# Kernel optimization log

Hardware: AMD Instinct MI355X
Metric: run time of the kernel (lower is better)

## Reference

```python
import jax, jax.numpy as jnp
import numpy as np
from jax import lax

B = 2; H = 32; W = 32; C = 384
NH = 12; NG = 6; KK = 7; STRIDE = 1; ORF = 2.0
CG = C // NG; HC = C // NH; GH = NH // NG; HID = 4 * C
EPS = 1e-5


def layernorm(x, w, b):
    mu = jnp.mean(x, axis=-1, keepdims=True)
    var = jnp.mean((x - mu) ** 2, axis=-1, keepdims=True)
    return (x - mu) * lax.rsqrt(var + EPS) * w + b


def ref_points(Hk, Wk):
    # normalized reference grid in (-1,1), ordering (y, x) as in _get_ref_points
    ry = ((jnp.arange(Hk, dtype=jnp.float32) + 0.5) / Hk) * 2.0 - 1.0
    rx = ((jnp.arange(Wk, dtype=jnp.float32) + 0.5) / Wk) * 2.0 - 1.0
    return jnp.stack(jnp.meshgrid(ry, rx, indexing='ij'), axis=-1)  # (Hk, Wk, 2)


def grid_sample(img, grid):
    # torch F.grid_sample: bilinear, align_corners=True, padding_mode='zeros'
    # img: (N, Cc, Hi, Wi); grid: (N, ..., 2) with (x, y) in [-1, 1]
    N, Cc, Hi, Wi = img.shape
    out_shape = grid.shape[1:-1]
    g = grid.reshape(N, -1, 2)
    x = (g[..., 0] + 1.0) * 0.5 * (Wi - 1)
    y = (g[..., 1] + 1.0) * 0.5 * (Hi - 1)
    x0 = jnp.floor(x); y0 = jnp.floor(y)
    wx1 = x - x0; wy1 = y - y0
    flat = img.reshape(N, Cc, Hi * Wi)
    M = g.shape[1]
    def gather(ix, iy, wgt):
        valid = (ix >= 0) & (ix <= Wi - 1) & (iy >= 0) & (iy <= Hi - 1)
        idx = (jnp.clip(iy, 0, Hi - 1) * Wi + jnp.clip(ix, 0, Wi - 1)).astype(jnp.int32)
        vals = jnp.take_along_axis(flat, jnp.broadcast_to(idx[:, None, :], (N, Cc, M)), axis=2)
        return vals * (wgt * valid.astype(img.dtype))[:, None, :]
    out = (gather(x0, y0, (1 - wx1) * (1 - wy1))
           + gather(x0 + 1, y0, wx1 * (1 - wy1))
           + gather(x0, y0 + 1, (1 - wx1) * wy1)
           + gather(x0 + 1, y0 + 1, wx1 * wy1))
    return out.reshape((N, Cc) + out_shape)


def setup_inputs() -> dict:
    ks = jax.random.split(jax.random.key(0), 16)
    n = lambda k, s, sc=0.02: jax.random.normal(k, s, jnp.float32) * sc
    return dict(
        x=jax.random.normal(ks[0], (B, H * W, C), jnp.float32),
        norm1_w=jnp.ones((C,), jnp.float32), norm1_b=jnp.zeros((C,), jnp.float32),
        wq=n(ks[1], (C, C)), bq=jnp.zeros((C,), jnp.float32),
        wk=n(ks[2], (C, C)), bk=jnp.zeros((C,), jnp.float32),
        wv=n(ks[3], (C, C)), bv=jnp.zeros((C,), jnp.float32),
        wo=n(ks[4], (C, C)), bo=jnp.zeros((C,), jnp.float32),
        off_dw_w=n(ks[5], (CG, 1, KK, KK)), off_dw_b=jnp.zeros((CG,), jnp.float32),
        off_ln_w=jnp.ones((CG,), jnp.float32), off_ln_b=jnp.zeros((CG,), jnp.float32),
        off_pw_w=n(ks[6], (2, CG)),
        rpe_table=n(ks[7], (NH, 2 * H - 1, 2 * W - 1), 0.01),
        norm2_w=jnp.ones((C,), jnp.float32), norm2_b=jnp.zeros((C,), jnp.float32),
        fc1_w=n(ks[8], (HID, C)), fc1_b=jnp.zeros((HID,), jnp.float32),
        fc2_w=n(ks[9], (C, HID)), fc2_b=jnp.zeros((C,), jnp.float32),
    )


def reference(x, norm1_w, norm1_b, wq, bq, wk, bk, wv, bv, wo, bo,
              off_dw_w, off_dw_b, off_ln_w, off_ln_b, off_pw_w, rpe_table,
              norm2_w, norm2_b, fc1_w, fc1_b, fc2_w, fc2_b):
    Bx, L, Cx = x.shape
    shortcut = x
    xn = layernorm(x, norm1_w, norm1_b)
    xi = xn.reshape(Bx, H, W, Cx).transpose(0, 3, 1, 2)  # (B, C, H, W)

    # proj_q (1x1 conv)
    q = jnp.einsum('bchw,dc->bdhw', xi, wq) + bq[None, :, None, None]

    # offset network on per-group channels
    q_off = q.reshape(Bx * NG, CG, H, W)
    o = lax.conv_general_dilated(q_off, off_dw_w, (STRIDE, STRIDE),
                                 [(KK // 2, KK // 2), (KK // 2, KK // 2)],
                                 dimension_numbers=('NCHW', 'OIHW', 'NCHW'),
                                 feature_group_count=CG) + off_dw_b[None, :, None, None]
    o = layernorm(o.transpose(0, 2, 3, 1), off_ln_w, off_ln_b)  # (Bg, Hk, Wk, CG)
    o = jax.nn.gelu(o, approximate=False)
    offset = jnp.einsum('bhwc,pc->bphw', o, off_pw_w)  # (Bg, 2, Hk, Wk)
    Hk, Wk = offset.shape[2], offset.shape[3]
    ns = Hk * Wk
    orange = jnp.array([1.0 / Hk, 1.0 / Wk], jnp.float32).reshape(1, 2, 1, 1)
    offset = jnp.tanh(offset) * orange * ORF
    offset = offset.transpose(0, 2, 3, 1)  # (Bg, Hk, Wk, 2) (y, x)
    pos = offset + ref_points(Hk, Wk)[None]  # offset_range_factor >= 0 branch

    # deformable sampling of the (normed) feature map
    xs = grid_sample(xi.reshape(Bx * NG, CG, H, W), pos[..., ::-1])  # (Bg, CG, Hk, Wk)
    xs = xs.reshape(Bx, Cx, 1, ns)

    k = (jnp.einsum('bcxn,dc->bdxn', xs, wk) + bk[None, :, None, None]).reshape(Bx * NH, HC, ns)
    v = (jnp.einsum('bcxn,dc->bdxn', xs, wv) + bv[None, :, None, None]).reshape(Bx * NH, HC, ns)
    q_ = q.reshape(Bx * NH, HC, H * W)

    attn = jnp.einsum('bcm,bcn->bmn', q_, k) * (HC ** -0.5)  # (B*NH, HW, ns)

    # continuous relative position bias via grid_sample on rpe_table
    rpe = jnp.broadcast_to(rpe_table[None], (Bx, NH, 2 * H - 1, 2 * W - 1)).reshape(
        Bx * NG, GH, 2 * H - 1, 2 * W - 1)
    qg = ref_points(H, W).reshape(H * W, 2)[None]  # (1, HW, 2)
    disp = (qg[:, :, None, :] - pos.reshape(Bx * NG, ns, 2)[:, None, :, :]) * 0.5  # (Bg, HW, ns, 2)
    bias = grid_sample(rpe, disp[..., ::-1])  # (Bg, GH, HW, ns)
    attn = attn + bias.reshape(Bx * NH, H * W, ns)

    attn = jax.nn.softmax(attn, axis=2)
    out = jnp.einsum('bmn,bcn->bcm', attn, v).reshape(Bx, Cx, H, W)
    y = jnp.einsum('bchw,dc->bdhw', out, wo) + bo[None, :, None, None]
    y = y.transpose(0, 2, 3, 1).reshape(Bx, L, Cx)

    x2 = shortcut + y
    h = layernorm(x2, norm2_w, norm2_b)
    h = jax.nn.gelu(h @ fc1_w.T + fc1_b, approximate=False) @ fc2_w.T + fc2_b
    return x2 + h
```

## Files before the change

### kernel.cpp

```cpp
#include <hip/hip_runtime.h>
#include <math.h>

#define Bc 2
#define Hh 32
#define Ww 32
#define Cc 384
#define NHc 12
#define NGc 6
#define CGc 64
#define HCc 32
#define GHc 2
#define HIDc 1536
#define Lc 1024
#define NSc 1024
#define BGc 12

typedef float f32x4 __attribute__((ext_vector_type(4)));
typedef short bf16x8 __attribute__((ext_vector_type(8)));

__device__ __forceinline__ float gelu_f(float v) {
    return 0.5f * v * (1.f + erff(v * 0.70710678118654752440f));
}

__device__ __forceinline__ unsigned short f2bf(float f) {
    unsigned u = __float_as_uint(f);
    u = (u + 0x7FFF + ((u >> 16) & 1)) >> 16;
    return (unsigned short)u;
}

__device__ __forceinline__ float bf2f(unsigned short u) {
    return __uint_as_float((unsigned)u << 16);
}

__global__ __launch_bounds__(128) void ln_kernel(
    const float* __restrict__ x, const float* __restrict__ w,
    const float* __restrict__ b, unsigned short* __restrict__ out)
{
    __shared__ float l1[2], l2[2];
    int row = blockIdx.x;
    int t = threadIdx.x;
    const float* xr = x + (size_t)row * Cc;
    float v0 = xr[t], v1 = xr[t + 128], v2 = xr[t + 256];
    float s = v0 + v1 + v2;
    #pragma unroll
    for (int o = 32; o; o >>= 1) s += __shfl_down(s, o);
    if ((t & 63) == 0) l1[t >> 6] = s;
    __syncthreads();
    float mu = (l1[0] + l1[1]) * (1.f / Cc);
    float d0 = v0 - mu, d1 = v1 - mu, d2 = v2 - mu;
    float q = d0 * d0 + d1 * d1 + d2 * d2;
    #pragma unroll
    for (int o = 32; o; o >>= 1) q += __shfl_down(q, o);
    if ((t & 63) == 0) l2[t >> 6] = q;
    __syncthreads();
    float rstd = rsqrtf((l2[0] + l2[1]) * (1.f / Cc) + 1e-5f);
    unsigned short* orow = out + (size_t)row * Cc;
    orow[t]       = f2bf(d0 * rstd * w[t]       + b[t]);
    orow[t + 128] = f2bf(d1 * rstd * w[t + 128] + b[t + 128]);
    orow[t + 256] = f2bf(d2 * rstd * w[t + 256] + b[t + 256]);
}

__global__ __launch_bounds__(256) void cast_kernel(
    const float* __restrict__ src, unsigned short* __restrict__ dst, int n)
{
    int i = blockIdx.x * 1024 + threadIdx.x * 4;
    if (i < n) {
        float4 v = *(const float4*)(src + i);
        ushort4 u;
        u.x = f2bf(v.x); u.y = f2bf(v.y); u.z = f2bf(v.z); u.w = f2bf(v.w);
        *(ushort4*)(dst + i) = u;
    }
}

template<int EPI>
__global__ __launch_bounds__(256) void mfma_gemm(
    const unsigned short* __restrict__ A, const unsigned short* __restrict__ W,
    const float* __restrict__ bias, const float* __restrict__ res,
    void* __restrict__ out1, void* __restrict__ out2, int M, int N, int K)
{
    int w = threadIdx.x >> 6, l = threadIdx.x & 63;
    int col = l & 15, quad = l >> 4;
    int mb = blockIdx.x * 64 + w * 16;
    int n0 = blockIdx.y * 64;
    const unsigned short* Ap = A + (size_t)(mb + col) * K + quad * 8;
    f32x4 acc[4] = {};
    for (int k0 = 0; k0 < K; k0 += 32) {
        bf16x8 af = *(const bf16x8*)(Ap + k0);
        #pragma unroll
        for (int ch = 0; ch < 4; ch++) {
            bf16x8 wf = *(const bf16x8*)(W + (size_t)(n0 + ch * 16 + col) * K + k0 + quad * 8);
            acc[ch] = __builtin_amdgcn_mfma_f32_16x16x32_bf16(af, wf, acc[ch], 0, 0, 0);
        }
    }
    int bb = mb >> 10, l0 = (mb & 1023) + quad * 4;
    #pragma unroll
    for (int ch = 0; ch < 4; ch++) {
        int n = n0 + ch * 16 + col;
        float bv = bias[n];
        if (EPI == 3) {
            float4 qv;
            qv.x = acc[ch][0] + bv; qv.y = acc[ch][1] + bv;
            qv.z = acc[ch][2] + bv; qv.w = acc[ch][3] + bv;
            *(float4*)&((float*)out1)[((size_t)(bb * Cc + n)) * Lc + l0] = qv;
            unsigned short* q2 = (unsigned short*)out2;
            size_t base = (((size_t)(bb * NHc + (n >> 5))) * Lc + l0) * 32 + (n & 31);
            q2[base]      = f2bf(qv.x);
            q2[base + 32] = f2bf(qv.y);
            q2[base + 64] = f2bf(qv.z);
            q2[base + 96] = f2bf(qv.w);
        } else if (EPI == 5) {
            ushort4 u;
            u.x = f2bf(acc[ch][0] + bv); u.y = f2bf(acc[ch][1] + bv);
            u.z = f2bf(acc[ch][2] + bv); u.w = f2bf(acc[ch][3] + bv);
            *(ushort4*)&((unsigned short*)out1)[((size_t)(bb * Cc + n)) * NSc + l0] = u;
        } else {
            #pragma unroll
            for (int r = 0; r < 4; r++) {
                size_t m = mb + quad * 4 + r;
                float v = acc[ch][r] + bv;
                if (EPI == 1)
                    ((unsigned short*)out1)[m * N + n] = f2bf(gelu_f(v));
                else if (EPI == 4)
                    ((unsigned short*)out1)[m * N + n] = f2bf(v);
                else
                    ((float*)out1)[m * N + n] = v + res[m * N + n];
            }
        }
    }
}

__global__ __launch_bounds__(256) void dwconv_kernel(
    const float* __restrict__ q, const float* __restrict__ wdw,
    const float* __restrict__ bdw, float* __restrict__ o_dw)
{
    int cg = blockIdx.x, bg = blockIdx.y;
    int b = bg / NGc, g = bg % NGc;
    __shared__ float wk_s[49];
    __shared__ float img[1024];
    const float* qp = q + (size_t)(b * Cc + g * CGc + cg) * Lc;
    if (threadIdx.x < 49) wk_s[threadIdx.x] = wdw[cg * 49 + threadIdx.x];
    #pragma unroll
    for (int i = 0; i < 4; i++) img[threadIdx.x + i * 256] = qp[threadIdx.x + i * 256];
    __syncthreads();
    float bias = bdw[cg];
    #pragma unroll
    for (int i = 0; i < 4; i++) {
        int hw = threadIdx.x + i * 256;
        int y = hw >> 5, xx = hw & 31;
        float acc = bias;
        #pragma unroll
        for (int ky = 0; ky < 7; ky++) {
            int yy = y + ky - 3;
            if (yy < 0 || yy > 31) continue;
            #pragma unroll
            for (int kx = 0; kx < 7; kx++) {
                int x2 = xx + kx - 3;
                if (x2 < 0 || x2 > 31) continue;
                acc += img[yy * 32 + x2] * wk_s[ky * 7 + kx];
            }
        }
        o_dw[(size_t)(bg * CGc + cg) * Lc + hw] = acc;
    }
}

__global__ __launch_bounds__(64) void offset_kernel(
    const float* __restrict__ o_dw, const float* __restrict__ lnw,
    const float* __restrict__ lnb, const float* __restrict__ pw,
    float* __restrict__ pos)
{
    int hw = blockIdx.x, bg = blockIdx.y;
    int cg = threadIdx.x;
    float v = o_dw[(size_t)(bg * CGc + cg) * Lc + hw];
    float s = v;
    #pragma unroll
    for (int o = 32; o; o >>= 1) s += __shfl_down(s, o);
    s = __shfl(s, 0, 64);
    float mu = s * (1.f / CGc);
    float d = v - mu;
    float q2 = d * d;
    #pragma unroll
    for (int o = 32; o; o >>= 1) q2 += __shfl_down(q2, o);
    q2 = __shfl(q2, 0, 64);
    float rstd = rsqrtf(q2 * (1.f / CGc) + 1e-5f);
    float t = d * rstd * lnw[cg] + lnb[cg];
    float gl = gelu_f(t);
    float sy = gl * pw[cg];
    float sx = gl * pw[CGc + cg];
    #pragma unroll
    for (int o = 32; o; o >>= 1) {
        sy += __shfl_down(sy, o);
        sx += __shfl_down(sx, o);
    }
    if (threadIdx.x == 0) {
        float offy = tanhf(sy) * 0.0625f;
        float offx = tanhf(sx) * 0.0625f;
        int y = hw >> 5, xx = hw & 31;
        pos[((size_t)bg * Lc + hw) * 2 + 0] = offy + ((y + 0.5f) * (2.f / Hh) - 1.f);
        pos[((size_t)bg * Lc + hw) * 2 + 1] = offx + ((xx + 0.5f) * (2.f / Ww) - 1.f);
    }
}

__global__ __launch_bounds__(256) void sample_kernel(
    const unsigned short* __restrict__ xn, const float* __restrict__ pos,
    unsigned short* __restrict__ xs)
{
    int cg = threadIdx.x & 63;
    int nl = threadIdx.x >> 6;
    int n = blockIdx.x * 4 + nl;
    int bg = blockIdx.y;
    int b = bg / NGc, g = bg % NGc;
    float py = pos[((size_t)bg * NSc + n) * 2 + 0];
    float px = pos[((size_t)bg * NSc + n) * 2 + 1];
    float fx = (px + 1.f) * 0.5f * 31.f;
    float fy = (py + 1.f) * 0.5f * 31.f;
    float x0f = floorf(fx), y0f = floorf(fy);
    int x0 = (int)x0f, y0 = (int)y0f;
    float wx1 = fx - x0f, wy1 = fy - y0f;
    float wx0 = 1.f - wx1, wy0 = 1.f - wy1;
    const unsigned short* base = xn + (size_t)(b * Lc) * Cc + g * CGc + cg;
    float acc = 0.f;
    if (y0 >= 0 && y0 <= 31) {
        if (x0 >= 0 && x0 <= 31) acc += bf2f(base[(size_t)(y0 * 32 + x0) * Cc]) * wx0 * wy0;
        if (x0 + 1 >= 0 && x0 + 1 <= 31) acc += bf2f(base[(size_t)(y0 * 32 + x0 + 1) * Cc]) * wx1 * wy0;
    }
    if (y0 + 1 >= 0 && y0 + 1 <= 31) {
        if (x0 >= 0 && x0 <= 31) acc += bf2f(base[(size_t)((y0 + 1) * 32 + x0) * Cc]) * wx0 * wy1;
        if (x0 + 1 >= 0 && x0 + 1 <= 31) acc += bf2f(base[(size_t)((y0 + 1) * 32 + x0 + 1) * Cc]) * wx1 * wy1;
    }
    xs[((size_t)(b * NSc) + n) * Cc + g * CGc + cg] = f2bf(acc);
}

__global__ __launch_bounds__(256) void attn_kernel(
    const unsigned short* __restrict__ qbf, const unsigned short* __restrict__ kbf,
    const unsigned short* __restrict__ vtb, const float* __restrict__ pos,
    const float* __restrict__ rpe, unsigned short* __restrict__ attno)
{
    __shared__ float rpe_s[63 * 65];
    __shared__ unsigned short p_bf[4][16 * 72];
    __shared__ float ml_s[4][2][16];
    float* o_s = rpe_s;

    int m0 = blockIdx.x * 16;
    int h = blockIdx.y, b = blockIdx.z;
    int tid = threadIdx.x;
    int w = tid >> 6, l = tid & 63;
    int col = l & 15, quad = l >> 4;

    const float* tb = rpe + (size_t)h * 3969;
    for (int i = tid; i < 63 * 65; i += 256) {
        int row = i / 65, cx = i - row * 65;
        rpe_s[i] = (cx < 63) ? tb[row * 63 + cx] : 0.f;
    }

    bf16x8 qfrag = *(const bf16x8*)(qbf +
        ((((size_t)(b * NHc + h)) * Lc + m0 + col) * 32 + quad * 8));

    float qgy = ((m0 >> 5) + 0.5f) * (2.f / 32.f) - 1.f;
    float qgx0 = (((m0 & 31) + quad * 4) + 0.5f) * (2.f / 32.f) - 1.f;

    const unsigned short* kb_ = kbf + (size_t)b * NSc * Cc + h * HCc;
    const unsigned short* vb_ = vtb + ((size_t)(b * Cc + h * HCc)) * NSc;
    const float2* pp = (const float2*)(pos + (size_t)(b * NGc + (h >> 1)) * NSc * 2);

    float run_m[4] = {-3.0e38f, -3.0e38f, -3.0e38f, -3.0e38f};
    float run_l[4] = {0.f, 0.f, 0.f, 0.f};
    f32x4 O0 = {0.f, 0.f, 0.f, 0.f};
    f32x4 O1 = {0.f, 0.f, 0.f, 0.f};

    __syncthreads();

    for (int it = 0; it < 4; it++) {
        int n0 = w * 256 + it * 64;
        f32x4 s[4];
        #pragma unroll
        for (int ch = 0; ch < 4; ch++) {
            bf16x8 kf = *(const bf16x8*)(kb_ +
                ((size_t)(n0 + ch * 16 + col) * Cc + quad * 8));
            f32x4 z = {0.f, 0.f, 0.f, 0.f};
            s[ch] = __builtin_amdgcn_mfma_f32_16x16x32_bf16(qfrag, kf, z, 0, 0, 0);
        }
        #pragma unroll
        for (int ch = 0; ch < 4; ch++) {
            int n = n0 + ch * 16 + col;
            float2 pyx = pp[n];
            float fy = ((qgy - pyx.x) * 0.5f + 1.f) * 31.f;
            float y0f = floorf(fy);
            int iy = (int)y0f;
            float wy1 = fy - y0f, wy0 = 1.f - wy1;
            bool y0ok = (unsigned)iy <= 62u;
            bool y1ok = (unsigned)(iy + 1) <= 62u;
            const float* r0 = rpe_s + iy * 65;
            float fx0 = ((qgx0 - pyx.y) * 0.5f + 1.f) * 31.f;
            #pragma unroll
            for (int r = 0; r < 4; r++) {
                float fx = fx0 + r * 0.96875f;
                float x0f = floorf(fx);
                int ix = (int)x0f;
                float wx1 = fx - x0f, wx0 = 1.f - wx1;
                bool x0ok = (unsigned)ix <= 62u;
                bool x1ok = (unsigned)(ix + 1) <= 62u;
                float bias = 0.f;
                if (y0ok) {
                    if (x0ok) bias += r0[ix] * wy0 * wx0;
                    if (x1ok) bias += r0[ix + 1] * wy0 * wx1;
                }
                if (y1ok) {
                    if (x0ok) bias += r0[65 + ix] * wy1 * wx0;
                    if (x1ok) bias += r0[65 + ix + 1] * wy1 * wx1;
                }
                s[ch][r] = s[ch][r] * 0.17677669529663688f + bias;
            }
        }
        float nm[4], alpha[4];
        #pragma unroll
        for (int r = 0; r < 4; r++) {
            float mx = fmaxf(fmaxf(s[0][r], s[1][r]), fmaxf(s[2][r], s[3][r]));
            #pragma unroll
            for (int msk = 1; msk < 16; msk <<= 1)
                mx = fmaxf(mx, __shfl_xor(mx, msk));
            nm[r] = fmaxf(run_m[r], mx);
            alpha[r] = expf(run_m[r] - nm[r]);
            run_m[r] = nm[r];
        }
        float rowsum[4] = {0.f, 0.f, 0.f, 0.f};
        #pragma unroll
        for (int ch = 0; ch < 4; ch++)
            #pragma unroll
            for (int r = 0; r < 4; r++) {
                float e = expf(s[ch][r] - nm[r]);
                s[ch][r] = e;
                rowsum[r] += e;
            }
        #pragma unroll
        for (int r = 0; r < 4; r++) {
            float sm = rowsum[r];
            #pragma unroll
            for (int msk = 1; msk < 16; msk <<= 1)
                sm += __shfl_xor(sm, msk);
            run_l[r] = run_l[r] * alpha[r] + sm;
        }
        #pragma unroll
        for (int ch = 0; ch < 4; ch++)
            #pragma unroll
            for (int r = 0; r < 4; r++)
                p_bf[w][(quad * 4 + r) * 72 + ch * 16 + col] = f2bf(s[ch][r]);
        #pragma unroll
        for (int r = 0; r < 4; r++) { O0[r] *= alpha[r]; O1[r] *= alpha[r]; }
        #pragma unroll
        for (int half = 0; half < 2; half++) {
            bf16x8 pf = *(const bf16x8*)&p_bf[w][col * 72 + half * 32 + quad * 8];
            bf16x8 v0 = *(const bf16x8*)(vb_ +
                ((size_t)col * NSc + n0 + half * 32 + quad * 8));
            O0 = __builtin_amdgcn_mfma_f32_16x16x32_bf16(pf, v0, O0, 0, 0, 0);
            bf16x8 v1 = *(const bf16x8*)(vb_ +
                ((size_t)(col + 16) * NSc + n0 + half * 32 + quad * 8));
            O1 = __builtin_amdgcn_mfma_f32_16x16x32_bf16(pf, v1, O1, 0, 0, 0);
        }
    }
    __syncthreads();
    #pragma unroll
    for (int r = 0; r < 4; r++) {
        int m = quad * 4 + r;
        o_s[w * 528 + m * 33 + col] = O0[r];
        o_s[w * 528 + m * 33 + col + 16] = O1[r];
    }
    if (col == 0) {
        #pragma unroll
        for (int r = 0; r < 4; r++) {
            ml_s[w][0][quad * 4 + r] = run_m[r];
            ml_s[w][1][quad * 4 + r] = run_l[r];
        }
    }
    __syncthreads();
    for (int i = tid; i < 512; i += 256) {
        int m = i >> 5, c = i & 31;
        float fm = fmaxf(fmaxf(ml_s[0][0][m], ml_s[1][0][m]),
                         fmaxf(ml_s[2][0][m], ml_s[3][0][m]));
        float lsum = 0.f, osum = 0.f;
        #pragma unroll
        for (int ww = 0; ww < 4; ww++) {
            float sc = expf(ml_s[ww][0][m] - fm);
            lsum += ml_s[ww][1][m] * sc;
            osum += o_s[ww * 528 + m * 33 + c] * sc;
        }
        attno[((size_t)(b * Lc) + m0 + m) * Cc + h * HCc + c] = f2bf(osum / lsum);
    }
}

extern "C" void kernel_launch(void* const* d_in, const int* in_sizes, int n_in,
                              void* d_out, int out_size, void* d_ws, size_t ws_size,
                              hipStream_t stream)
{
    const float* x    = (const float*)d_in[0];
    const float* n1w  = (const float*)d_in[1];
    const float* n1b  = (const float*)d_in[2];
    const float* wq   = (const float*)d_in[3];
    const float* bq   = (const float*)d_in[4];
    const float* wk   = (const float*)d_in[5];
    const float* bk   = (const float*)d_in[6];
    const float* wv   = (const float*)d_in[7];
    const float* bv   = (const float*)d_in[8];
    const float* wo   = (const float*)d_in[9];
    const float* bo   = (const float*)d_in[10];
    const float* dw_w = (const float*)d_in[11];
    const float* dw_b = (const float*)d_in[12];
    const float* lnw  = (const float*)d_in[13];
    const float* lnb  = (const float*)d_in[14];
    const float* pw_w = (const float*)d_in[15];
    const float* rpe  = (const float*)d_in[16];
    const float* n2w  = (const float*)d_in[17];
    const float* n2b  = (const float*)d_in[18];
    const float* fc1w = (const float*)d_in[19];
    const float* fc1b = (const float*)d_in[20];
    const float* fc2w = (const float*)d_in[21];
    const float* fc2b = (const float*)d_in[22];
    float* out = (float*)d_out;

    float* ws = (float*)d_ws;
    unsigned short* xnbf = (unsigned short*)ws;
    float*          qb   = ws + 393216;
    unsigned short* qbf  = (unsigned short*)(ws + 1179648);
    unsigned short* h1bf = (unsigned short*)ws;
    float* odw   = ws + 1572864;
    unsigned short* xln2bf = (unsigned short*)(ws + 1572864);
    float* posb  = ws + 2359296;
    unsigned short* xsbf = (unsigned short*)(ws + 2383872);
    unsigned short* kbf  = (unsigned short*)(ws + 2777088);
    unsigned short* vtb  = (unsigned short*)(ws + 3170304);
    unsigned short* attnbf = (unsigned short*)(ws + 3563520);
    float* x2    = ws + 3956736;
    unsigned short* wqbf   = (unsigned short*)(ws + 4743168);
    unsigned short* wkbf   = (unsigned short*)(ws + 4816896);
    unsigned short* wvbf   = (unsigned short*)(ws + 4890624);
    unsigned short* wobf   = (unsigned short*)(ws + 4964352);
    unsigned short* fc1wbf = (unsigned short*)(ws + 5038080);
    unsigned short* fc2wbf = (unsigned short*)(ws + 5332992);

    cast_kernel<<<(Cc * Cc + 1023) / 1024, 256, 0, stream>>>(wq, wqbf, Cc * Cc);
    cast_kernel<<<(Cc * Cc + 1023) / 1024, 256, 0, stream>>>(wk, wkbf, Cc * Cc);
    cast_kernel<<<(Cc * Cc + 1023) / 1024, 256, 0, stream>>>(wv, wvbf, Cc * Cc);
    cast_kernel<<<(Cc * Cc + 1023) / 1024, 256, 0, stream>>>(wo, wobf, Cc * Cc);
    cast_kernel<<<(Cc * HIDc + 1023) / 1024, 256, 0, stream>>>(fc1w, fc1wbf, Cc * HIDc);
    cast_kernel<<<(Cc * HIDc + 1023) / 1024, 256, 0, stream>>>(fc2w, fc2wbf, Cc * HIDc);
    ln_kernel<<<Bc * Lc, 128, 0, stream>>>(x, n1w, n1b, xnbf);
    mfma_gemm<3><<<dim3(Bc * Lc / 64, Cc / 64), 256, 0, stream>>>(
        xnbf, wqbf, bq, x, qb, qbf, Bc * Lc, Cc, Cc);
    dwconv_kernel<<<dim3(CGc, BGc), 256, 0, stream>>>(qb, dw_w, dw_b, odw);
    offset_kernel<<<dim3(Lc, BGc), 64, 0, stream>>>(odw, lnw, lnb, pw_w, posb);
    sample_kernel<<<dim3(NSc / 4, BGc), 256, 0, stream>>>(xnbf, posb, xsbf);
    mfma_gemm<4><<<dim3(Bc * NSc / 64, Cc / 64), 256, 0, stream>>>(
        xsbf, wkbf, bk, x, kbf, kbf, Bc * NSc, Cc, Cc);
    mfma_gemm<5><<<dim3(Bc * NSc / 64, Cc / 64), 256, 0, stream>>>(
        xsbf, wvbf, bv, x, vtb, vtb, Bc * NSc, Cc, Cc);
    attn_kernel<<<dim3(Lc / 16, NHc, Bc), 256, 0, stream>>>(
        qbf, kbf, vtb, posb, rpe, attnbf);
    mfma_gemm<2><<<dim3(Bc * Lc / 64, Cc / 64), 256, 0, stream>>>(
        attnbf, wobf, bo, x, x2, x2, Bc * Lc, Cc, Cc);
    ln_kernel<<<Bc * Lc, 128, 0, stream>>>(x2, n2w, n2b, xln2bf);
    mfma_gemm<1><<<dim3(Bc * Lc / 64, HIDc / 64), 256, 0, stream>>>(
        xln2bf, fc1wbf, fc1b, x2, h1bf, h1bf, Bc * Lc, HIDc, Cc);
    mfma_gemm<2><<<dim3(Bc * Lc / 64, Cc / 64), 256, 0, stream>>>(
        h1bf, fc2wbf, fc2b, x2, out, out, Bc * Lc, Cc, HIDc);
}
```

Measured before the change: 331.8 us.

## Fuse weight casts and K/V GEMMs, narrow GEMM tiles, bf16 exp2 RPE table

Merges the six weight-cast launches into one kernel and fuses the K and V projections into a single MFMA kernel that shares the A-fragment load. Generic GEMM N-tiles are halved to 32 columns to double the grid, and offset_kernel now packs four positions per 256-thread block. The attention kernel stores the RPE table in shared memory as bf16 pre-scaled by log2(e) and uses exp2f, cutting LDS footprint and exp cost. The bf16 RPE values add some precision loss in the bias.

```diff
diff --git a/kernel.cpp b/kernel.cpp
--- a/kernel.cpp
+++ b/kernel.cpp
@@ -60,16 +60,27 @@
     orow[t + 256] = f2bf(d2 * rstd * w[t + 256] + b[t + 256]);
 }
 
-__global__ __launch_bounds__(256) void cast_kernel(
-    const float* __restrict__ src, unsigned short* __restrict__ dst, int n)
-{
-    int i = blockIdx.x * 1024 + threadIdx.x * 4;
-    if (i < n) {
-        float4 v = *(const float4*)(src + i);
-        ushort4 u;
-        u.x = f2bf(v.x); u.y = f2bf(v.y); u.z = f2bf(v.z); u.w = f2bf(v.w);
-        *(ushort4*)(dst + i) = u;
-    }
+__global__ __launch_bounds__(256) void cast6_kernel(
+    const float* __restrict__ wq, const float* __restrict__ wk,
+    const float* __restrict__ wv, const float* __restrict__ wo,
+    const float* __restrict__ f1, const float* __restrict__ f2,
+    unsigned short* __restrict__ dq, unsigned short* __restrict__ dk,
+    unsigned short* __restrict__ dv, unsigned short* __restrict__ d_o,
+    unsigned short* __restrict__ d1, unsigned short* __restrict__ d2)
+{
+    int bid = blockIdx.x;
+    const float* s; unsigned short* d; int base;
+    if (bid < 144)       { s = wq; d = dq;  base = bid; }
+    else if (bid < 288)  { s = wk; d = dk;  base = bid - 144; }
+    else if (bid < 432)  { s = wv; d = dv;  base = bid - 288; }
+    else if (bid < 576)  { s = wo; d = d_o; base = bid - 432; }
+    else if (bid < 1152) { s = f1; d = d1;  base = bid - 576; }
+    else                 { s = f2; d = d2;  base = bid - 1152; }
+    int i = base * 1024 + threadIdx.x * 4;
+    float4 v = *(const float4*)(s + i);
+    ushort4 u;
+    u.x = f2bf(v.x); u.y = f2bf(v.y); u.z = f2bf(v.z); u.w = f2bf(v.w);
+    *(ushort4*)(d + i) = u;
 }
 
 template<int EPI>
@@ -81,20 +92,22 @@
     int w = threadIdx.x >> 6, l = threadIdx.x & 63;
     int col = l & 15, quad = l >> 4;
     int mb = blockIdx.x * 64 + w * 16;
-    int n0 = blockIdx.y * 64;
+    int n0 = blockIdx.y * 32;
     const unsigned short* Ap = A + (size_t)(mb + col) * K + quad * 8;
-    f32x4 acc[4] = {};
+    const unsigned short* Wp0 = W + (size_t)(n0 + col) * K + quad * 8;
+    const unsigned short* Wp1 = W + (size_t)(n0 + 16 + col) * K + quad * 8;
+    f32x4 acc[2] = {};
+    #pragma unroll 4
     for (int k0 = 0; k0 < K; k0 += 32) {
         bf16x8 af = *(const bf16x8*)(Ap + k0);
-        #pragma unroll
-        for (int ch = 0; ch < 4; ch++) {
-            bf16x8 wf = *(const bf16x8*)(W + (size_t)(n0 + ch * 16 + col) * K + k0 + quad * 8);
-            acc[ch] = __builtin_amdgcn_mfma_f32_16x16x32_bf16(af, wf, acc[ch], 0, 0, 0);
-        }
+        bf16x8 w0 = *(const bf16x8*)(Wp0 + k0);
+        bf16x8 w1 = *(const bf16x8*)(Wp1 + k0);
+        acc[0] = __builtin_amdgcn_mfma_f32_16x16x32_bf16(af, w0, acc[0], 0, 0, 0);
+        acc[1] = __builtin_amdgcn_mfma_f32_16x16x32_bf16(af, w1, acc[1], 0, 0, 0);
     }
     int bb = mb >> 10, l0 = (mb & 1023) + quad * 4;
     #pragma unroll
-    for (int ch = 0; ch < 4; ch++) {
+    for (int ch = 0; ch < 2; ch++) {
         int n = n0 + ch * 16 + col;
         float bv = bias[n];
         if (EPI == 3) {
@@ -108,11 +121,6 @@
             q2[base + 32] = f2bf(qv.y);
             q2[base + 64] = f2bf(qv.z);
             q2[base + 96] = f2bf(qv.w);
-        } else if (EPI == 5) {
-            ushort4 u;
-            u.x = f2bf(acc[ch][0] + bv); u.y = f2bf(acc[ch][1] + bv);
-            u.z = f2bf(acc[ch][2] + bv); u.w = f2bf(acc[ch][3] + bv);
-            *(ushort4*)&((unsigned short*)out1)[((size_t)(bb * Cc + n)) * NSc + l0] = u;
         } else {
             #pragma unroll
             for (int r = 0; r < 4; r++) {
@@ -120,12 +128,53 @@
                 float v = acc[ch][r] + bv;
                 if (EPI == 1)
                     ((unsigned short*)out1)[m * N + n] = f2bf(gelu_f(v));
-                else if (EPI == 4)
-                    ((unsigned short*)out1)[m * N + n] = f2bf(v);
                 else
                     ((float*)out1)[m * N + n] = v + res[m * N + n];
             }
         }
+    }
+}
+
+__global__ __launch_bounds__(256) void mfma_kv(
+    const unsigned short* __restrict__ A, const unsigned short* __restrict__ Wk,
+    const unsigned short* __restrict__ Wv, const float* __restrict__ bk,
+    const float* __restrict__ bv, unsigned short* __restrict__ kout,
+    unsigned short* __restrict__ vout, int M, int K)
+{
+    int w = threadIdx.x >> 6, l = threadIdx.x & 63;
+    int col = l & 15, quad = l >> 4;
+    int mb = blockIdx.x * 64 + w * 16;
+    int n0 = blockIdx.y * 32;
+    const unsigned short* Ap = A + (size_t)(mb + col) * K + quad * 8;
+    const unsigned short* Wk0 = Wk + (size_t)(n0 + col) * K + quad * 8;
+    const unsigned short* Wk1 = Wk + (size_t)(n0 + 16 + col) * K + quad * 8;
+    const unsigned short* Wv0 = Wv + (size_t)(n0 + col) * K + quad * 8;
+    const unsigned short* Wv1 = Wv + (size_t)(n0 + 16 + col) * K + quad * 8;
+    f32x4 ak[2] = {}, av[2] = {};
+    #pragma unroll 4
+    for (int k0 = 0; k0 < K; k0 += 32) {
+        bf16x8 af = *(const bf16x8*)(Ap + k0);
+        bf16x8 k0f = *(const bf16x8*)(Wk0 + k0);
+        bf16x8 k1f = *(const bf16x8*)(Wk1 + k0);
+        bf16x8 v0f = *(const bf16x8*)(Wv0 + k0);
+        bf16x8 v1f = *(const bf16x8*)(Wv1 + k0);
+        ak[0] = __builtin_amdgcn_mfma_f32_16x16x32_bf16(af, k0f, ak[0], 0, 0, 0);
+        ak[1] = __builtin_amdgcn_mfma_f32_16x16x32_bf16(af, k1f, ak[1], 0, 0, 0);
+        av[0] = __builtin_amdgcn_mfma_f32_16x16x32_bf16(af, v0f, av[0], 0, 0, 0);
+        av[1] = __builtin_amdgcn_mfma_f32_16x16x32_bf16(af, v1f, av[1], 0, 0, 0);
+    }
+    int bb = mb >> 10, l0 = (mb & 1023) + quad * 4;
+    #pragma unroll
+    for (int ch = 0; ch < 2; ch++) {
+        int n = n0 + ch * 16 + col;
+        float bkv = bk[n], bvv = bv[n];
+        #pragma unroll
+        for (int r = 0; r < 4; r++)
+            kout[(size_t)(mb + quad * 4 + r) * Cc + n] = f2bf(ak[ch][r] + bkv);
+        ushort4 u;
+        u.x = f2bf(av[ch][0] + bvv); u.y = f2bf(av[ch][1] + bvv);
+        u.z = f2bf(av[ch][2] + bvv); u.w = f2bf(av[ch][3] + bvv);
+        *(ushort4*)&vout[((size_t)(bb * Cc + n)) * NSc + l0] = u;
     }
 }
 
@@ -163,13 +212,14 @@
     }
 }
 
-__global__ __launch_bounds__(64) void offset_kernel(
+__global__ __launch_bounds__(256) void offset_kernel(
     const float* __restrict__ o_dw, const float* __restrict__ lnw,
     const float* __restrict__ lnb, const float* __restrict__ pw,
     float* __restrict__ pos)
 {
-    int hw = blockIdx.x, bg = blockIdx.y;
-    int cg = threadIdx.x;
+    int hw = blockIdx.x * 4 + (threadIdx.x >> 6);
+    int bg = blockIdx.y;
+    int cg = threadIdx.x & 63;
     float v = o_dw[(size_t)(bg * CGc + cg) * Lc + hw];
     float s = v;
     #pragma unroll
@@ -191,7 +241,7 @@
         sy += __shfl_down(sy, o);
         sx += __shfl_down(sx, o);
     }
-    if (threadIdx.x == 0) {
+    if (cg == 0) {
         float offy = tanhf(sy) * 0.0625f;
         float offx = tanhf(sx) * 0.0625f;
         int y = hw >> 5, xx = hw & 31;
@@ -235,10 +285,10 @@
     const unsigned short* __restrict__ vtb, const float* __restrict__ pos,
     const float* __restrict__ rpe, unsigned short* __restrict__ attno)
 {
-    __shared__ float rpe_s[63 * 65];
+    __shared__ float o_smem[2112];
     __shared__ unsigned short p_bf[4][16 * 72];
     __shared__ float ml_s[4][2][16];
-    float* o_s = rpe_s;
+    unsigned short* rpe_s = (unsigned short*)o_smem;
 
     int m0 = blockIdx.x * 16;
     int h = blockIdx.y, b = blockIdx.z;
@@ -249,7 +299,7 @@
     const float* tb = rpe + (size_t)h * 3969;
     for (int i = tid; i < 63 * 65; i += 256) {
         int row = i / 65, cx = i - row * 65;
-        rpe_s[i] = (cx < 63) ? tb[row * 63 + cx] : 0.f;
+        rpe_s[i] = (cx < 63) ? f2bf(tb[row * 63 + cx] * 1.44269504f) : 0;
     }
 
     bf16x8 qfrag = *(const bf16x8*)(qbf +
@@ -289,7 +339,7 @@
             float wy1 = fy - y0f, wy0 = 1.f - wy1;
             bool y0ok = (unsigned)iy <= 62u;
             bool y1ok = (unsigned)(iy + 1) <= 62u;
-            const float* r0 = rpe_s + iy * 65;
+            const unsigned short* r0 = rpe_s + iy * 65;
             float fx0 = ((qgx0 - pyx.y) * 0.5f + 1.f) * 31.f;
             #pragma unroll
             for (int r = 0; r < 4; r++) {
@@ -301,14 +351,14 @@
                 bool x1ok = (unsigned)(ix + 1) <= 62u;
                 float bias = 0.f;
                 if (y0ok) {
-                    if (x0ok) bias += r0[ix] * wy0 * wx0;
-                    if (x1ok) bias += r0[ix + 1] * wy0 * wx1;
+                    if (x0ok) bias += bf2f(r0[ix]) * wy0 * wx0;
+                    if (x1ok) bias += bf2f(r0[ix + 1]) * wy0 * wx1;
                 }
                 if (y1ok) {
-                    if (x0ok) bias += r0[65 + ix] * wy1 * wx0;
-                    if (x1ok) bias += r0[65 + ix + 1] * wy1 * wx1;
+                    if (x0ok) bias += bf2f(r0[65 + ix]) * wy1 * wx0;
+                    if (x1ok) bias += bf2f(r0[65 + ix + 1]) * wy1 * wx1;
                 }
-                s[ch][r] = s[ch][r] * 0.17677669529663688f + bias;
+                s[ch][r] = s[ch][r] * 0.25506974f + bias;
             }
         }
         float nm[4], alpha[4];
@@ -319,7 +369,7 @@
             for (int msk = 1; msk < 16; msk <<= 1)
                 mx = fmaxf(mx, __shfl_xor(mx, msk));
             nm[r] = fmaxf(run_m[r], mx);
-            alpha[r] = expf(run_m[r] - nm[r]);
+            alpha[r] = exp2f(run_m[r] - nm[r]);
             run_m[r] = nm[r];
         }
         float rowsum[4] = {0.f, 0.f, 0.f, 0.f};
@@ -327,7 +377,7 @@
         for (int ch = 0; ch < 4; ch++)
             #pragma unroll
             for (int r = 0; r < 4; r++) {
-                float e = expf(s[ch][r] - nm[r]);
+                float e = exp2f(s[ch][r] - nm[r]);
                 s[ch][r] = e;
                 rowsum[r] += e;
             }
@@ -358,6 +408,7 @@
         }
     }
     __syncthreads();
+    float* o_s = o_smem;
     #pragma unroll
     for (int r = 0; r < 4; r++) {
         int m = quad * 4 + r;
@@ -379,7 +430,7 @@
         float lsum = 0.f, osum = 0.f;
         #pragma unroll
         for (int ww = 0; ww < 4; ww++) {
-            float sc = expf(ml_s[ww][0][m] - fm);
+            float sc = exp2f(ml_s[ww][0][m] - fm);
             lsum += ml_s[ww][1][m] * sc;
             osum += o_s[ww * 528 + m * 33 + c] * sc;
         }
@@ -436,29 +487,23 @@
     unsigned short* fc1wbf = (unsigned short*)(ws + 5038080);
     unsigned short* fc2wbf = (unsigned short*)(ws + 5332992);
 
-    cast_kernel<<<(Cc * Cc + 1023) / 1024, 256, 0, stream>>>(wq, wqbf, Cc * Cc);
-    cast_kernel<<<(Cc * Cc + 1023) / 1024, 256, 0, stream>>>(wk, wkbf, Cc * Cc);
-    cast_kernel<<<(Cc * Cc + 1023) / 1024, 256, 0, stream>>>(wv, wvbf, Cc * Cc);
-    cast_kernel<<<(Cc * Cc + 1023) / 1024, 256, 0, stream>>>(wo, wobf, Cc * Cc);
-    cast_kernel<<<(Cc * HIDc + 1023) / 1024, 256, 0, stream>>>(fc1w, fc1wbf, Cc * HIDc);
-    cast_kernel<<<(Cc * HIDc + 1023) / 1024, 256, 0, stream>>>(fc2w, fc2wbf, Cc * HIDc);
+    cast6_kernel<<<1728, 256, 0, stream>>>(
+        wq, wk, wv, wo, fc1w, fc2w, wqbf, wkbf, wvbf, wobf, fc1wbf, fc2wbf);
     ln_kernel<<<Bc * Lc, 128, 0, stream>>>(x, n1w, n1b, xnbf);
-    mfma_gemm<3><<<dim3(Bc * Lc / 64, Cc / 64), 256, 0, stream>>>(
+    mfma_gemm<3><<<dim3(Bc * Lc / 64, Cc / 32), 256, 0, stream>>>(
         xnbf, wqbf, bq, x, qb, qbf, Bc * Lc, Cc, Cc);
     dwconv_kernel<<<dim3(CGc, BGc), 256, 0, stream>>>(qb, dw_w, dw_b, odw);
-    offset_kernel<<<dim3(Lc, BGc), 64, 0, stream>>>(odw, lnw, lnb, pw_w, posb);
+    offset_kernel<<<dim3(Lc / 4, BGc), 256, 0, stream>>>(odw, lnw, lnb, pw_w, posb);
     sample_kernel<<<dim3(NSc / 4, BGc), 256, 0, stream>>>(xnbf, posb, xsbf);
-    mfma_gemm<4><<<dim3(Bc * NSc / 64, Cc / 64), 256, 0, stream>>>(
-        xsbf, wkbf, bk, x, kbf, kbf, Bc * NSc, Cc, Cc);
-    mfma_gemm<5><<<dim3(Bc * NSc / 64, Cc / 64), 256, 0, stream>>>(
-        xsbf, wvbf, bv, x, vtb, vtb, Bc * NSc, Cc, Cc);
+    mfma_kv<<<dim3(Bc * NSc / 64, Cc / 32), 256, 0, stream>>>(
+        xsbf, wkbf, wvbf, bk, bv, kbf, vtb, Bc * NSc, Cc);
     attn_kernel<<<dim3(Lc / 16, NHc, Bc), 256, 0, stream>>>(
         qbf, kbf, vtb, posb, rpe, attnbf);
-    mfma_gemm<2><<<dim3(Bc * Lc / 64, Cc / 64), 256, 0, stream>>>(
+    mfma_gemm<2><<<dim3(Bc * Lc / 64, Cc / 32), 256, 0, stream>>>(
         attnbf, wobf, bo, x, x2, x2, Bc * Lc, Cc, Cc);
     ln_kernel<<<Bc * Lc, 128, 0, stream>>>(x2, n2w, n2b, xln2bf);
-    mfma_gemm<1><<<dim3(Bc * Lc / 64, HIDc / 64), 256, 0, stream>>>(
+    mfma_gemm<1><<<dim3(Bc * Lc / 64, HIDc / 32), 256, 0, stream>>>(
         xln2bf, fc1wbf, fc1b, x2, h1bf, h1bf, Bc * Lc, HIDc, Cc);
-    mfma_gemm<2><<<dim3(Bc * Lc / 64, Cc / 64), 256, 0, stream>>>(
+    mfma_gemm<2><<<dim3(Bc * Lc / 64, Cc / 32), 256, 0, stream>>>(
         h1bf, fc2wbf, fc2b, x2, out, out, Bc * Lc, Cc, HIDc);
 }
```

After: 298.1 us. -10.2%, faster.
